# Optimization experiments

Measured on AMD Instinct MI355X. Metric: run time of the kernel, lower is better.

Reference implementation:

```python
import jax, jax.numpy as jnp
import numpy as np
from jax import lax

CROP = 4
DATA_RANGE = 255.0
KSIZE = 11


def _box_filter(x):
    # x: [B,1,H,W]; 11x11 uniform kernel, padding 5 (SAME), single channel
    k = jnp.ones((1, 1, KSIZE, KSIZE), dtype=x.dtype) / (KSIZE * KSIZE)
    return lax.conv_general_dilated(
        x, k, window_strides=(1, 1), padding=[(5, 5), (5, 5)],
        dimension_numbers=("NCHW", "OIHW", "NCHW"))


def setup_inputs() -> dict:
    key = jax.random.key(0)
    k1, k2 = jax.random.split(key)
    img1 = jax.random.uniform(k1, (16, 3, 512, 512), dtype=jnp.float32) * DATA_RANGE
    img2 = jax.random.uniform(k2, (16, 3, 512, 512), dtype=jnp.float32) * DATA_RANGE
    return {"img1": img1, "img2": img2}


def reference(img1, img2):
    # only_test_y_channel: take channel 0
    x1 = img1[:, 0:1, :, :]
    x2 = img2[:, 0:1, :, :]
    # crop_border = 4
    x1 = x1[:, :, CROP:-CROP, CROP:-CROP].astype(jnp.float32)
    x2 = x2[:, :, CROP:-CROP, CROP:-CROP].astype(jnp.float32)

    C1 = (0.01 * DATA_RANGE) ** 2
    C2 = (0.03 * DATA_RANGE) ** 2

    mu1 = _box_filter(x1)
    mu2 = _box_filter(x2)
    mu1_sq = mu1 * mu1
    mu2_sq = mu2 * mu2
    mu1_mu2 = mu1 * mu2
    sigma1_sq = _box_filter(x1 * x1) - mu1_sq
    sigma2_sq = _box_filter(x2 * x2) - mu2_sq
    sigma12 = _box_filter(x1 * x2) - mu1_mu2

    ssim_map = ((2 * mu1_mu2 + C1) * (2 * sigma12 + C2)) / (
        (mu1_sq + mu2_sq + C1) * (sigma1_sq + sigma2_sq + C2))
    return jnp.mean(ssim_map)
```

## Files before the change

### kernel.cpp

```cpp
#include <hip/hip_runtime.h>

#define CROPPX 4
#define H 504
#define W 504
#define IMG 512
#define NB 16
#define NCH 3
#define KS 11
#define RAD 5
#define TW 64
#define STRIP (TW + 2*RAD)
#define RPS 42
#define NSEG 12
#define NXT 8

__global__ __launch_bounds__(64) void ssim_main(const float* __restrict__ img1,
                                                const float* __restrict__ img2,
                                                double* __restrict__ partial) {
    const int tid = threadIdx.x;
    const int gx0 = blockIdx.x * TW;
    const int y0  = blockIdx.y * RPS;
    const int b   = blockIdx.z;
    const int nrows = (y0 + RPS <= H) ? RPS : (H - y0);

    __shared__ float rowA[STRIP];
    __shared__ float rowB[STRIP];
    __shared__ float hist[KS][5][TW];

    for (int i = tid; i < KS * 5 * TW; i += 64) ((float*)hist)[i] = 0.f;

    const float* p1 = img1 + (size_t)(b * NCH) * IMG * IMG;
    const float* p2 = img2 + (size_t)(b * NCH) * IMG * IMG;

    double vs1 = 0, vs2 = 0, vs11 = 0, vs22 = 0, vs12 = 0;
    double ssum = 0.0;
    const double C1 = 6.5025, C2 = 58.5225;
    const double inv121 = 1.0 / 121.0;
    const bool colValid = (gx0 + tid) < W;

    for (int iter = 0; iter < nrows + 2 * RAD; ++iter) {
        const int r = y0 - RAD + iter;
        __syncthreads();
        const bool rowIn = (r >= 0) && (r < H);
        for (int s = tid; s < STRIP; s += 64) {
            const int c = gx0 - RAD + s;
            float a = 0.f, bb = 0.f;
            if (rowIn && c >= 0 && c < W) {
                const size_t off = (size_t)(r + CROPPX) * IMG + (c + CROPPX);
                a  = p1[off];
                bb = p2[off];
            }
            rowA[s] = a;
            rowB[s] = bb;
        }
        __syncthreads();

        float h1 = 0, h2 = 0, h11 = 0, h22 = 0, h12 = 0;
        #pragma unroll
        for (int dx = 0; dx < KS; ++dx) {
            const float a = rowA[tid + dx];
            const float c = rowB[tid + dx];
            h1 += a;
            h2 += c;
            h11 = fmaf(a, a, h11);
            h22 = fmaf(c, c, h22);
            h12 = fmaf(a, c, h12);
        }

        const int ring = iter % KS;
        vs1  += (double)h1  - (double)hist[ring][0][tid];
        vs2  += (double)h2  - (double)hist[ring][1][tid];
        vs11 += (double)h11 - (double)hist[ring][2][tid];
        vs22 += (double)h22 - (double)hist[ring][3][tid];
        vs12 += (double)h12 - (double)hist[ring][4][tid];
        hist[ring][0][tid] = h1;
        hist[ring][1][tid] = h2;
        hist[ring][2][tid] = h11;
        hist[ring][3][tid] = h22;
        hist[ring][4][tid] = h12;

        if (iter >= 2 * RAD && colValid) {
            const double mu1 = vs1 * inv121;
            const double mu2 = vs2 * inv121;
            const double mu1s = mu1 * mu1;
            const double mu2s = mu2 * mu2;
            const double m12  = mu1 * mu2;
            const double s1  = vs11 * inv121 - mu1s;
            const double s2  = vs22 * inv121 - mu2s;
            const double s12 = vs12 * inv121 - m12;
            const double num = (2.0 * m12 + C1) * (2.0 * s12 + C2);
            const double den = (mu1s + mu2s + C1) * (s1 + s2 + C2);
            ssum += num / den;
        }
    }

    for (int off = 32; off > 0; off >>= 1)
        ssum += __shfl_down(ssum, off);
    if (tid == 0) {
        const int bidx = (blockIdx.z * gridDim.y + blockIdx.y) * gridDim.x + blockIdx.x;
        partial[bidx] = ssum;
    }
}

__global__ __launch_bounds__(256) void ssim_final(const double* __restrict__ partial,
                                                  int n, float* __restrict__ out) {
    __shared__ double sh[256];
    double s = 0.0;
    for (int i = threadIdx.x; i < n; i += 256) s += partial[i];
    sh[threadIdx.x] = s;
    __syncthreads();
    for (int stride = 128; stride > 0; stride >>= 1) {
        if (threadIdx.x < stride) sh[threadIdx.x] += sh[threadIdx.x + stride];
        __syncthreads();
    }
    if (threadIdx.x == 0)
        out[0] = (float)(sh[0] / ((double)NB * (double)H * (double)W));
}

extern "C" void kernel_launch(void* const* d_in, const int* in_sizes, int n_in,
                              void* d_out, int out_size, void* d_ws, size_t ws_size,
                              hipStream_t stream) {
    const float* img1 = (const float*)d_in[0];
    const float* img2 = (const float*)d_in[1];
    float* out = (float*)d_out;
    double* partial = (double*)d_ws;

    dim3 grid(NXT, NSEG, NB);
    ssim_main<<<grid, 64, 0, stream>>>(img1, img2, partial);
    ssim_final<<<1, 256, 0, stream>>>(partial, NXT * NSEG * NB, out);
}
```

Before: 162.6 us.

## Switch SSIM to float math, register ring buffer, prefetch rows, more segments

Replaces the double-precision running sums and SSIM formula with fp32, which removes slow fp64 arithmetic and divides. The shared-memory history ring becomes a fully unrolled register ring indexed by compile-time position. The next row's global loads are issued before the current row is computed, and the two images are interleaved in shared memory as float2. Rows per block drop from 42 to 28 to launch more blocks. fp32 running sums with add/subtract can drift and lose accuracy, and the register ring raises register pressure.

```diff
diff --git a/kernel.cpp b/kernel.cpp
--- a/kernel.cpp
+++ b/kernel.cpp
@@ -10,87 +10,98 @@
 #define RAD 5
 #define TW 64
 #define STRIP (TW + 2*RAD)
-#define RPS 42
-#define NSEG 12
+#define RPS 28
+#define NSEG 18
 #define NXT 8
+#define TOTAL (RPS + 2*RAD)
 
 __global__ __launch_bounds__(64) void ssim_main(const float* __restrict__ img1,
                                                 const float* __restrict__ img2,
-                                                double* __restrict__ partial) {
+                                                float* __restrict__ partial) {
     const int tid = threadIdx.x;
     const int gx0 = blockIdx.x * TW;
     const int y0  = blockIdx.y * RPS;
     const int b   = blockIdx.z;
-    const int nrows = (y0 + RPS <= H) ? RPS : (H - y0);
 
-    __shared__ float rowA[STRIP];
-    __shared__ float rowB[STRIP];
-    __shared__ float hist[KS][5][TW];
+    __shared__ float2 rowAB[STRIP];
 
-    for (int i = tid; i < KS * 5 * TW; i += 64) ((float*)hist)[i] = 0.f;
+    const float* p1 = img1 + (size_t)(b * NCH) * IMG * IMG + (size_t)CROPPX * IMG + CROPPX;
+    const float* p2 = img2 + (size_t)(b * NCH) * IMG * IMG + (size_t)CROPPX * IMG + CROPPX;
 
-    const float* p1 = img1 + (size_t)(b * NCH) * IMG * IMG;
-    const float* p2 = img2 + (size_t)(b * NCH) * IMG * IMG;
+    float r1[KS], r2[KS], r11[KS], r22[KS], r12[KS];
+    #pragma unroll
+    for (int j = 0; j < KS; ++j) { r1[j]=0.f; r2[j]=0.f; r11[j]=0.f; r22[j]=0.f; r12[j]=0.f; }
 
-    double vs1 = 0, vs2 = 0, vs11 = 0, vs22 = 0, vs12 = 0;
-    double ssum = 0.0;
-    const double C1 = 6.5025, C2 = 58.5225;
-    const double inv121 = 1.0 / 121.0;
+    float vs1 = 0.f, vs2 = 0.f, vs11 = 0.f, vs22 = 0.f, vs12 = 0.f;
+    float ssum = 0.f;
+    const float C1 = 6.5025f, C2 = 58.5225f;
+    const float inv121 = 1.0f / 121.0f;
     const bool colValid = (gx0 + tid) < W;
+    const int c0 = gx0 - RAD + tid;
+    const int c1 = c0 + 64;
+    const bool lane2 = tid < (STRIP - 64);
 
-    for (int iter = 0; iter < nrows + 2 * RAD; ++iter) {
-        const int r = y0 - RAD + iter;
-        __syncthreads();
-        const bool rowIn = (r >= 0) && (r < H);
-        for (int s = tid; s < STRIP; s += 64) {
-            const int c = gx0 - RAD + s;
-            float a = 0.f, bb = 0.f;
-            if (rowIn && c >= 0 && c < W) {
-                const size_t off = (size_t)(r + CROPPX) * IMG + (c + CROPPX);
-                a  = p1[off];
-                bb = p2[off];
+    float a0 = 0.f, b0 = 0.f, a1 = 0.f, b1 = 0.f;
+    {
+        const int r = y0 - RAD;
+        if ((unsigned)r < (unsigned)H) {
+            const size_t ro = (size_t)r * IMG;
+            if ((unsigned)c0 < (unsigned)W) { a0 = p1[ro + c0]; b0 = p2[ro + c0]; }
+            if (lane2 && (unsigned)c1 < (unsigned)W) { a1 = p1[ro + c1]; b1 = p2[ro + c1]; }
+        }
+    }
+
+    for (int base = 0; base < TOTAL; base += KS) {
+        #pragma unroll
+        for (int j = 0; j < KS; ++j) {
+            const int iter = base + j;
+            if (iter >= TOTAL) break;
+
+            __syncthreads();
+            rowAB[tid] = make_float2(a0, b0);
+            if (lane2) rowAB[64 + tid] = make_float2(a1, b1);
+            __syncthreads();
+
+            a0 = 0.f; b0 = 0.f; a1 = 0.f; b1 = 0.f;
+            if (iter + 1 < TOTAL) {
+                const int rn = y0 - RAD + iter + 1;
+                if ((unsigned)rn < (unsigned)H) {
+                    const size_t ro = (size_t)rn * IMG;
+                    if ((unsigned)c0 < (unsigned)W) { a0 = p1[ro + c0]; b0 = p2[ro + c0]; }
+                    if (lane2 && (unsigned)c1 < (unsigned)W) { a1 = p1[ro + c1]; b1 = p2[ro + c1]; }
+                }
             }
-            rowA[s] = a;
-            rowB[s] = bb;
-        }
-        __syncthreads();
 
-        float h1 = 0, h2 = 0, h11 = 0, h22 = 0, h12 = 0;
-        #pragma unroll
-        for (int dx = 0; dx < KS; ++dx) {
-            const float a = rowA[tid + dx];
-            const float c = rowB[tid + dx];
-            h1 += a;
-            h2 += c;
-            h11 = fmaf(a, a, h11);
-            h22 = fmaf(c, c, h22);
-            h12 = fmaf(a, c, h12);
-        }
+            float h1 = 0.f, h2 = 0.f, h11 = 0.f, h22 = 0.f, h12 = 0.f;
+            #pragma unroll
+            for (int dx = 0; dx < KS; ++dx) {
+                const float2 ab = rowAB[tid + dx];
+                h1 += ab.x;
+                h2 += ab.y;
+                h11 = fmaf(ab.x, ab.x, h11);
+                h22 = fmaf(ab.y, ab.y, h22);
+                h12 = fmaf(ab.x, ab.y, h12);
+            }
 
-        const int ring = iter % KS;
-        vs1  += (double)h1  - (double)hist[ring][0][tid];
-        vs2  += (double)h2  - (double)hist[ring][1][tid];
-        vs11 += (double)h11 - (double)hist[ring][2][tid];
-        vs22 += (double)h22 - (double)hist[ring][3][tid];
-        vs12 += (double)h12 - (double)hist[ring][4][tid];
-        hist[ring][0][tid] = h1;
-        hist[ring][1][tid] = h2;
-        hist[ring][2][tid] = h11;
-        hist[ring][3][tid] = h22;
-        hist[ring][4][tid] = h12;
+            vs1  += h1  - r1[j];  r1[j]  = h1;
+            vs2  += h2  - r2[j];  r2[j]  = h2;
+            vs11 += h11 - r11[j]; r11[j] = h11;
+            vs22 += h22 - r22[j]; r22[j] = h22;
+            vs12 += h12 - r12[j]; r12[j] = h12;
 
-        if (iter >= 2 * RAD && colValid) {
-            const double mu1 = vs1 * inv121;
-            const double mu2 = vs2 * inv121;
-            const double mu1s = mu1 * mu1;
-            const double mu2s = mu2 * mu2;
-            const double m12  = mu1 * mu2;
-            const double s1  = vs11 * inv121 - mu1s;
-            const double s2  = vs22 * inv121 - mu2s;
-            const double s12 = vs12 * inv121 - m12;
-            const double num = (2.0 * m12 + C1) * (2.0 * s12 + C2);
-            const double den = (mu1s + mu2s + C1) * (s1 + s2 + C2);
-            ssum += num / den;
+            if (iter >= 2 * RAD && colValid) {
+                const float mu1 = vs1 * inv121;
+                const float mu2 = vs2 * inv121;
+                const float mu1s = mu1 * mu1;
+                const float mu2s = mu2 * mu2;
+                const float m12  = mu1 * mu2;
+                const float s1  = fmaf(vs11, inv121, -mu1s);
+                const float s2  = fmaf(vs22, inv121, -mu2s);
+                const float s12 = fmaf(vs12, inv121, -m12);
+                const float num = (2.0f * m12 + C1) * (2.0f * s12 + C2);
+                const float den = (mu1s + mu2s + C1) * (s1 + s2 + C2);
+                ssum += num / den;
+            }
         }
     }
 
@@ -102,11 +113,11 @@
     }
 }
 
-__global__ __launch_bounds__(256) void ssim_final(const double* __restrict__ partial,
+__global__ __launch_bounds__(256) void ssim_final(const float* __restrict__ partial,
                                                   int n, float* __restrict__ out) {
     __shared__ double sh[256];
     double s = 0.0;
-    for (int i = threadIdx.x; i < n; i += 256) s += partial[i];
+    for (int i = threadIdx.x; i < n; i += 256) s += (double)partial[i];
     sh[threadIdx.x] = s;
     __syncthreads();
     for (int stride = 128; stride > 0; stride >>= 1) {
@@ -123,7 +134,7 @@
     const float* img1 = (const float*)d_in[0];
     const float* img2 = (const float*)d_in[1];
     float* out = (float*)d_out;
-    double* partial = (double*)d_ws;
+    float* partial = (float*)d_ws;
 
     dim3 grid(NXT, NSEG, NB);
     ssim_main<<<grid, 64, 0, stream>>>(img1, img2, partial);
```

Measured after the change: 132.1 us. -18.7%, faster.
